# Kernel tuning notes

Hardware: AMD Instinct MI355X
Metric: run time of the kernel (lower is better)

## Reference

```python
import jax, jax.numpy as jnp
import numpy as np

B, TQ, TK, DQ, DK = 8, 2048, 2048, 512, 512


def setup_inputs() -> dict:
    key = jax.random.key(0)
    kq, kk, kv, km, kw = jax.random.split(key, 5)
    q = jax.random.normal(kq, (B, TQ, DQ), dtype=jnp.float32)
    k = jax.random.normal(kk, (B, TK, DK), dtype=jnp.float32)
    v = jax.random.normal(kv, (B, TK, DK), dtype=jnp.float32)
    attn_mask = jax.random.randint(km, (B, TQ, TK), 0, 2) > 0
    # xavier_uniform for (DQ, DK)
    limit = float(np.sqrt(6.0 / (DQ + DK)))
    weights = jax.random.uniform(kw, (DQ, DK), minval=-limit, maxval=limit, dtype=jnp.float32)
    return {"q": q, "k": k, "v": v, "attn_mask": attn_mask, "weights": weights}


def reference(q, k, v, attn_mask, weights):
    # scores: (B, TQ, TK) = (q @ W) @ k^T
    qw = jnp.einsum('bqd,de->bqe', q, weights)
    scores = jnp.einsum('bqe,bke->bqk', qw, k)
    scores = jnp.where(attn_mask, -jnp.inf, scores)
    attention = jax.nn.softmax(scores, axis=-1)
    # dropout_rate = 0.0 -> identity
    output = jnp.einsum('bqk,bkd->bqd', attention, v)
    return (output, attention)
```

## Files before the change

kernel.cpp:

```cpp
#include <hip/hip_runtime.h>
#include <stdint.h>

#define TQs 2048
#define TKs 2048
#define DDs 512
#define NBs 8

typedef float f32x4 __attribute__((ext_vector_type(4)));
typedef short bf16x8 __attribute__((ext_vector_type(8)));
typedef short bf16x4 __attribute__((ext_vector_type(4)));
typedef _Float16 half8 __attribute__((ext_vector_type(8)));

__device__ __forceinline__ unsigned short f2bf(float x){
  unsigned u = __float_as_uint(x);
  return (unsigned short)((u + 0x7fffu + ((u>>16)&1u)) >> 16);
}
__device__ __forceinline__ float bf2f(unsigned short h){
  return __uint_as_float(((unsigned)h)<<16);
}

__device__ __forceinline__ void gload16(const void* g, void* l){
  __builtin_amdgcn_global_load_lds(
      (const __attribute__((address_space(1))) unsigned int*)(unsigned long long)(uintptr_t)g,
      (__attribute__((address_space(3))) unsigned int*)(unsigned int)(uintptr_t)l,
      16, 0, 0);
}

__global__ __launch_bounds__(256) void k0_kf(const float* __restrict__ kk, _Float16* __restrict__ kf){
  const long n8 = (long)NBs*TKs*DDs/8;
  for(long i = (long)blockIdx.x*256 + threadIdx.x; i < n8; i += (long)gridDim.x*256){
    f32x4 x0 = ((const f32x4*)kk)[2*i];
    f32x4 x1 = ((const f32x4*)kk)[2*i+1];
    half8 h;
    #pragma unroll
    for(int j=0;j<4;j++){ h[j] = (_Float16)x0[j]; h[4+j] = (_Float16)x1[j]; }
    ((half8*)kf)[i] = h;
  }
}

__global__ __launch_bounds__(256) void k0_transpose_v(const float* __restrict__ v, short* __restrict__ vt){
  __shared__ float tile[64][65];
  int b = blockIdx.z;
  int t0 = blockIdx.x*64, d0 = blockIdx.y*64;
  int tid = threadIdx.x;
  int r = tid>>2, cs = (tid&3)*16;
  const float* src = v + ((long)b*TKs + t0 + r)*DDs + d0 + cs;
  #pragma unroll
  for(int i=0;i<4;i++){
    f32x4 x = ((const f32x4*)src)[i];
    tile[r][cs+4*i+0]=x[0]; tile[r][cs+4*i+1]=x[1]; tile[r][cs+4*i+2]=x[2]; tile[r][cs+4*i+3]=x[3];
  }
  __syncthreads();
  int dr = tid>>2, ts = (tid&3)*16;
  bf16x8 b0, b1;
  #pragma unroll
  for(int i=0;i<8;i++){ b0[i] = (short)f2bf(tile[ts+i][dr]); b1[i] = (short)f2bf(tile[ts+8+i][dr]); }
  short* dst = vt + ((long)b*DDs + d0 + dr)*TKs + t0 + ts;
  ((bf16x8*)dst)[0] = b0;
  ((bf16x8*)dst)[1] = b1;
}

__global__ __launch_bounds__(256) void k0_wt(const float* __restrict__ wsrc,
                                             short* __restrict__ wth, short* __restrict__ wtl){
  __shared__ float tile[64][65];
  int d0 = blockIdx.x*64, e0 = blockIdx.y*64;
  int tid = threadIdx.x;
  int r = tid>>2, cs = (tid&3)*16;
  const float* src = wsrc + ((long)(d0 + r))*DDs + e0 + cs;
  #pragma unroll
  for(int i=0;i<4;i++){
    f32x4 x = ((const f32x4*)src)[i];
    tile[r][cs+4*i+0]=x[0]; tile[r][cs+4*i+1]=x[1]; tile[r][cs+4*i+2]=x[2]; tile[r][cs+4*i+3]=x[3];
  }
  __syncthreads();
  int er = tid>>2, ds = (tid&3)*16;
  bf16x8 h0,h1,l0,l1;
  #pragma unroll
  for(int i=0;i<8;i++){
    float x = tile[ds+i][er];
    unsigned short hh = f2bf(x);
    h0[i] = (short)hh; l0[i] = (short)f2bf(x - bf2f(hh));
  }
  #pragma unroll
  for(int i=0;i<8;i++){
    float x = tile[ds+8+i][er];
    unsigned short hh = f2bf(x);
    h1[i] = (short)hh; l1[i] = (short)f2bf(x - bf2f(hh));
  }
  short* dh = wth + ((long)(e0+er))*DDs + d0 + ds;
  short* dl = wtl + ((long)(e0+er))*DDs + d0 + ds;
  ((bf16x8*)dh)[0] = h0; ((bf16x8*)dh)[1] = h1;
  ((bf16x8*)dl)[0] = l0; ((bf16x8*)dl)[1] = l1;
}

__global__ __launch_bounds__(256,2) void k1_qw(const float* __restrict__ q,
                                               const short* __restrict__ wth, const short* __restrict__ wtl,
                                               _Float16* __restrict__ qwh, _Float16* __restrict__ qwl){
  __shared__ short qah[8192], qal[8192];
  __shared__ short wbh[8192], wbl[8192];
  int q0 = blockIdx.x*128, e0 = blockIdx.y*128;
  int tid = threadIdx.x, lane = tid&63, w4 = tid>>6;
  int wm = w4>>1, wn = w4&1;
  int i15 = lane&15, g4 = lane>>4;
  f32x4 acc[4][4];
  #pragma unroll
  for(int a=0;a<4;a++)
    #pragma unroll
    for(int bq=0;bq<4;bq++) acc[a][bq] = (f32x4){0.f,0.f,0.f,0.f};
  for(int k0=0;k0<DDs;k0+=64){
    __syncthreads();
    #pragma unroll
    for(int j=0;j<4;j++){
      int J = j*4 + w4;
      long so = (long)(e0 + (J>>1)*16 + i15)*DDs + k0 + ((J&1)*4 + g4)*8;
      gload16(wth + so, &wbh[J*512]);
      gload16(wtl + so, &wbl[J*512]);
    }
    #pragma unroll
    for(int j=0;j<4;j++){
      int c = j*256 + tid;
      int ci = c&15, cg = (c>>4)&3, cks = (c>>6)&1, crb = c>>7;
      const float* s = q + (long)(q0 + crb*16 + ci)*DDs + k0 + (cks*4+cg)*8;
      f32x4 x0 = ((const f32x4*)s)[0];
      f32x4 x1 = ((const f32x4*)s)[1];
      bf16x8 h, l;
      #pragma unroll
      for(int jj=0;jj<4;jj++){
        unsigned short hj = f2bf(x0[jj]);
        h[jj] = (short)hj; l[jj] = (short)f2bf(x0[jj]-bf2f(hj));
      }
      #pragma unroll
      for(int jj=0;jj<4;jj++){
        unsigned short hj = f2bf(x1[jj]);
        h[4+jj] = (short)hj; l[4+jj] = (short)f2bf(x1[jj]-bf2f(hj));
      }
      *(bf16x8*)&qah[c*8] = h;
      *(bf16x8*)&qal[c*8] = l;
    }
    __syncthreads();
    #pragma unroll
    for(int ks=0;ks<2;ks++){
      bf16x8 a_h[4], a_l[4], b_h[4], b_l[4];
      #pragma unroll
      for(int mf=0;mf<4;mf++){
        int c = ((wm*4+mf)*2+ks)*64 + lane;
        a_h[mf] = *(const bf16x8*)&qah[c*8];
        a_l[mf] = *(const bf16x8*)&qal[c*8];
      }
      #pragma unroll
      for(int nf=0;nf<4;nf++){
        int c = ((wn*4+nf)*2+ks)*64 + lane;
        b_h[nf] = *(const bf16x8*)&wbh[c*8];
        b_l[nf] = *(const bf16x8*)&wbl[c*8];
      }
      #pragma unroll
      for(int mf=0;mf<4;mf++)
      #pragma unroll
      for(int nf=0;nf<4;nf++){
        acc[mf][nf] = __builtin_amdgcn_mfma_f32_16x16x32_bf16(a_h[mf], b_h[nf], acc[mf][nf],0,0,0);
        acc[mf][nf] = __builtin_amdgcn_mfma_f32_16x16x32_bf16(a_h[mf], b_l[nf], acc[mf][nf],0,0,0);
        acc[mf][nf] = __builtin_amdgcn_mfma_f32_16x16x32_bf16(a_l[mf], b_h[nf], acc[mf][nf],0,0,0);
      }
    }
  }
  int rr = g4*4, cc = i15;
  #pragma unroll
  for(int mf=0;mf<4;mf++)
  #pragma unroll
  for(int nf=0;nf<4;nf++)
  #pragma unroll
  for(int r2=0;r2<4;r2++){
    long row = q0 + wm*64 + mf*16 + rr + r2;
    long col = e0 + wn*64 + nf*16 + cc;
    float s = acc[mf][nf][r2];
    _Float16 h = (_Float16)s;
    qwh[row*DDs + col] = h;
    qwl[row*DDs + col] = (_Float16)(s - (float)h);
  }
}

__global__ __launch_bounds__(256,2) void k2a(const _Float16* __restrict__ qwh, const _Float16* __restrict__ qwl,
                                             const _Float16* __restrict__ kf,
                                             const int* __restrict__ mask, float* __restrict__ attn,
                                             float* __restrict__ m_ws, float* __restrict__ l_ws){
  __shared__ _Float16 kb[2][16384];
  int rb = blockIdx.x;
  int chunk = blockIdx.y;
  int tid = threadIdx.x, lane = tid&63, w = tid>>6;
  int b = rb>>5;
  long qrow0 = (long)rb*64 + w*16;
  int i15 = lane&15, g4 = lane>>4;
  half8 ah[16], al[16];
  {
    const _Float16* ph = qwh + (qrow0 + i15)*DDs + g4*8;
    const _Float16* pl = qwl + (qrow0 + i15)*DDs + g4*8;
    #pragma unroll
    for(int kc=0;kc<16;kc++){
      ah[kc] = *(const half8*)(ph + kc*32);
      al[kc] = *(const half8*)(pl + kc*32);
    }
  }
  float m_st[4], l_st[4];
  #pragma unroll
  for(int r=0;r<4;r++){ m_st[r]=-1e30f; l_st[r]=0.f; }
  const _Float16* kbase = kf + (long)b*TKs*DDs;
  {
    int t0 = chunk*512;
    #pragma unroll
    for(int j=0;j<8;j++){
      int J = j*4 + w;
      long so = (long)(t0 + ((J>>4)<<4) + i15)*DDs + (J&15)*32 + g4*8;
      gload16(kbase + so, &kb[0][J*512]);
    }
  }
  __syncthreads();
  int cur = 0;
  for(int it=0; it<16; ++it){
    int t0 = chunk*512 + it*32;
    if(it < 15){
      int t1 = t0 + 32;
      #pragma unroll
      for(int j=0;j<8;j++){
        int J = j*4 + w;
        long so = (long)(t1 + ((J>>4)<<4) + i15)*DDs + (J&15)*32 + g4*8;
        gload16(kbase + so, &kb[cur^1][J*512]);
      }
    }
    int mv[2][4];
    #pragma unroll
    for(int nf=0;nf<2;nf++)
      #pragma unroll
      for(int r=0;r<4;r++)
        mv[nf][r] = mask[(qrow0 + g4*4 + r)*TKs + t0 + nf*16 + i15];
    f32x4 acc[2];
    acc[0]=(f32x4){0.f,0.f,0.f,0.f}; acc[1]=(f32x4){0.f,0.f,0.f,0.f};
    #pragma unroll
    for(int ks=0;ks<16;ks++){
      #pragma unroll
      for(int nf=0;nf<2;nf++){
        half8 bh = *(const half8*)&kb[cur][((nf*16+ks)*64 + lane)*8];
        acc[nf] = __builtin_amdgcn_mfma_f32_16x16x32_f16(ah[ks], bh, acc[nf],0,0,0);
        acc[nf] = __builtin_amdgcn_mfma_f32_16x16x32_f16(al[ks], bh, acc[nf],0,0,0);
      }
    }
    #pragma unroll
    for(int r=0;r<4;r++){
      float s0 = acc[0][r];
      float s1 = acc[1][r];
      if(mv[0][r]) s0 = -3e38f;
      if(mv[1][r]) s1 = -3e38f;
      float mo = m_st[r];
      float mn = fmaxf(mo, fmaxf(s0,s1));
      l_st[r] = l_st[r]*__expf(mo-mn) + __expf(s0-mn) + __expf(s1-mn);
      m_st[r] = mn;
      long row = qrow0 + g4*4 + r;
      attn[row*TKs + t0 + i15] = s0;
      attn[row*TKs + t0 + 16 + i15] = s1;
    }
    __syncthreads();
    cur ^= 1;
  }
  #pragma unroll
  for(int r=0;r<4;r++){
    #pragma unroll
    for(int d=1; d<16; d<<=1){
      float m2 = __shfl_xor(m_st[r], d, 16);
      float l2 = __shfl_xor(l_st[r], d, 16);
      float mn = fmaxf(m_st[r], m2);
      l_st[r] = l_st[r]*__expf(m_st[r]-mn) + l2*__expf(m2-mn);
      m_st[r] = mn;
    }
  }
  if(i15==0){
    #pragma unroll
    for(int r=0;r<4;r++){
      long row = qrow0 + g4*4 + r;
      m_ws[row*4 + chunk] = m_st[r];
      l_ws[row*4 + chunk] = l_st[r];
    }
  }
}

__global__ __launch_bounds__(256,2) void k2b(const short* __restrict__ vt, const float* __restrict__ m_ws,
                                             const float* __restrict__ l_ws, float* __restrict__ attn,
                                             float* __restrict__ outp){
  __shared__ short vf[2][16384];
  __shared__ short at2[2][2048];
  __shared__ float ms[64], rls[64];
  int rb = blockIdx.x;
  long row0 = (long)rb*64;
  int b = rb>>5;
  int tid=threadIdx.x, lane=tid&63, w=tid>>6;
  int i15 = lane&15, g4 = lane>>4;
  const short* vb = vt + (long)b*DDs*TKs;
  float* arow = attn + row0*TKs;
  int r_ = tid>>2, t8w = tid&3;
  #pragma unroll
  for(int j=0;j<8;j++){
    int J = j*4 + w;
    long so = (long)(J*16 + i15)*TKs + g4*8;
    gload16(vb + so, &vf[0][J*512]);
  }
  if(tid < 64){
    long row = row0 + tid;
    float m0=m_ws[row*4+0], m1=m_ws[row*4+1], m2=m_ws[row*4+2], m3=m_ws[row*4+3];
    float M = fmaxf(fmaxf(m0,m1),fmaxf(m2,m3));
    float L = l_ws[row*4+0]*__expf(m0-M) + l_ws[row*4+1]*__expf(m1-M)
            + l_ws[row*4+2]*__expf(m2-M) + l_ws[row*4+3]*__expf(m3-M);
    ms[tid] = M;
    rls[tid] = 1.0f/L;
  }
  __syncthreads();
  {
    float* p = arow + (long)r_*TKs + t8w*8;
    f32x4 s0v = ((const f32x4*)p)[0];
    f32x4 s1v = ((const f32x4*)p)[1];
    float M = ms[r_], RL = rls[r_];
    f32x4 a0, a1;
    #pragma unroll
    for(int j=0;j<4;j++){ a0[j] = __expf(s0v[j]-M)*RL; a1[j] = __expf(s1v[j]-M)*RL; }
    ((f32x4*)p)[0] = a0;
    ((f32x4*)p)[1] = a1;
    bf16x8 ab;
    #pragma unroll
    for(int j=0;j<4;j++){ ab[j] = (short)f2bf(a0[j]); ab[4+j] = (short)f2bf(a1[j]); }
    int cell = ((r_>>4)<<6) + (t8w<<4) + (r_&15);
    *(bf16x8*)&at2[0][cell*8] = ab;
  }
  __syncthreads();
  f32x4 acc[4][8];
  #pragma unroll
  for(int mf=0;mf<4;mf++)
    #pragma unroll
    for(int nf=0;nf<8;nf++) acc[mf][nf]=(f32x4){0.f,0.f,0.f,0.f};
  int c = 0;
  for(int it=0; it<64; ++it){
    f32x4 s0v, s1v;
    if(it < 63){
      int t1 = (it+1)*32;
      #pragma unroll
      for(int j=0;j<8;j++){
        int J = j*4 + w;
        long so = (long)(J*16 + i15)*TKs + t1 + g4*8;
        gload16(vb + so, &vf[c^1][J*512]);
      }
      float* p = arow + (long)r_*TKs + t1 + t8w*8;
      s0v = ((const f32x4*)p)[0];
      s1v = ((const f32x4*)p)[1];
    }
    bf16x8 af[4], bfr[8];
    #pragma unroll
    for(int mf=0;mf<4;mf++) af[mf] = *(const bf16x8*)&at2[c][(mf*64 + lane)*8];
    #pragma unroll
    for(int nf=0;nf<8;nf++) bfr[nf] = *(const bf16x8*)&vf[c][((w*8+nf)*64 + lane)*8];
    #pragma unroll
    for(int mf=0;mf<4;mf++)
    #pragma unroll
    for(int nf=0;nf<8;nf++)
      acc[mf][nf] = __builtin_amdgcn_mfma_f32_16x16x32_bf16(af[mf], bfr[nf], acc[mf][nf],0,0,0);
    if(it < 63){
      int t1 = (it+1)*32;
      float* p = arow + (long)r_*TKs + t1 + t8w*8;
      float M = ms[r_], RL = rls[r_];
      f32x4 a0, a1;
      #pragma unroll
      for(int j=0;j<4;j++){ a0[j] = __expf(s0v[j]-M)*RL; a1[j] = __expf(s1v[j]-M)*RL; }
      ((f32x4*)p)[0] = a0;
      ((f32x4*)p)[1] = a1;
      bf16x8 ab;
      #pragma unroll
      for(int j=0;j<4;j++){ ab[j] = (short)f2bf(a0[j]); ab[4+j] = (short)f2bf(a1[j]); }
      int cell = ((r_>>4)<<6) + (t8w<<4) + (r_&15);
      *(bf16x8*)&at2[c^1][cell*8] = ab;
    }
    __syncthreads();
    c ^= 1;
  }
  #pragma unroll
  for(int mf=0;mf<4;mf++)
  #pragma unroll
  for(int nf=0;nf<8;nf++)
  #pragma unroll
  for(int r2=0;r2<4;r2++){
    long row = row0 + mf*16 + g4*4 + r2;
    long col = w*128 + nf*16 + i15;
    outp[row*DDs + col] = acc[mf][nf][r2];
  }
}

extern "C" void kernel_launch(void* const* d_in, const int* in_sizes, int n_in,
                              void* d_out, int out_size, void* d_ws, size_t ws_size,
                              hipStream_t stream) {
  const float* q    = (const float*)d_in[0];
  const float* k    = (const float*)d_in[1];
  const float* v    = (const float*)d_in[2];
  const int*   mask = (const int*)d_in[3];
  const float* wsrc = (const float*)d_in[4];
  float* outp = (float*)d_out;
  float* attn = (float*)d_out + (long)NBs*TQs*DDs;
  char* ws = (char*)d_ws;
  const long NE = (long)NBs*TKs*DDs;
  _Float16* kf  = (_Float16*)ws;
  short*    vt  = (short*)(ws + 2*NE);
  _Float16* qwh = (_Float16*)(ws + 4*NE);
  _Float16* qwl = (_Float16*)(ws + 6*NE);
  float* m_ws = (float*)(ws + 8*NE);
  float* l_ws = (float*)(ws + 8*NE + 65536*4);
  short* wth = (short*)attn;
  short* wtl = (short*)attn + 262144;
  hipLaunchKernelGGL(k0_kf,          dim3(1024),    dim3(256), 0, stream, k, kf);
  hipLaunchKernelGGL(k0_transpose_v, dim3(32,8,8),  dim3(256), 0, stream, v, vt);
  hipLaunchKernelGGL(k0_wt,          dim3(8,8),     dim3(256), 0, stream, wsrc, wth, wtl);
  hipLaunchKernelGGL(k1_qw,          dim3(128,4),   dim3(256), 0, stream, q, wth, wtl, qwh, qwl);
  hipLaunchKernelGGL(k2a,            dim3(256,4),   dim3(256), 0, stream, qwh, qwl, kf, mask, attn, m_ws, l_ws);
  hipLaunchKernelGGL(k2b,            dim3(256),     dim3(256), 0, stream, vt, m_ws, l_ws, attn, outp);
}
```

Measured before the change: 321.1 us.

## Shrink k2a key tile and split k2b into smaller row blocks for occupancy

k2a now processes 16 keys per iteration instead of 32, which halves its LDS tile and raises launch bounds to 3 blocks per CU. It keeps separate hi/lo accumulators to shorten the MFMA dependency chain. k2b now uses 32-row blocks with 512 threads and a grid of 512 blocks, so the grid covers more CUs and each warp holds fewer accumulators. The cost is more loop iterations and barriers in k2a, and V tiles reloaded by twice as many blocks in k2b.

Result: slower. 485.6 us (+51.2%).

```diff
diff --git a/kernel.cpp b/kernel.cpp
--- a/kernel.cpp
+++ b/kernel.cpp
@@ -179,11 +179,11 @@
   }
 }
 
-__global__ __launch_bounds__(256,2) void k2a(const _Float16* __restrict__ qwh, const _Float16* __restrict__ qwl,
+__global__ __launch_bounds__(256,3) void k2a(const _Float16* __restrict__ qwh, const _Float16* __restrict__ qwl,
                                              const _Float16* __restrict__ kf,
                                              const int* __restrict__ mask, float* __restrict__ attn,
                                              float* __restrict__ m_ws, float* __restrict__ l_ws){
-  __shared__ _Float16 kb[2][16384];
+  __shared__ _Float16 kb[2][8192];
   int rb = blockIdx.x;
   int chunk = blockIdx.y;
   int tid = threadIdx.x, lane = tid&63, w = tid>>6;
@@ -207,55 +207,46 @@
   {
     int t0 = chunk*512;
     #pragma unroll
-    for(int j=0;j<8;j++){
+    for(int j=0;j<4;j++){
       int J = j*4 + w;
-      long so = (long)(t0 + ((J>>4)<<4) + i15)*DDs + (J&15)*32 + g4*8;
+      long so = (long)(t0 + i15)*DDs + J*32 + g4*8;
       gload16(kbase + so, &kb[0][J*512]);
     }
   }
   __syncthreads();
   int cur = 0;
-  for(int it=0; it<16; ++it){
-    int t0 = chunk*512 + it*32;
-    if(it < 15){
-      int t1 = t0 + 32;
-      #pragma unroll
-      for(int j=0;j<8;j++){
+  for(int it=0; it<32; ++it){
+    int t0 = chunk*512 + it*16;
+    if(it < 31){
+      int t1 = t0 + 16;
+      #pragma unroll
+      for(int j=0;j<4;j++){
         int J = j*4 + w;
-        long so = (long)(t1 + ((J>>4)<<4) + i15)*DDs + (J&15)*32 + g4*8;
+        long so = (long)(t1 + i15)*DDs + J*32 + g4*8;
         gload16(kbase + so, &kb[cur^1][J*512]);
       }
     }
-    int mv[2][4];
-    #pragma unroll
-    for(int nf=0;nf<2;nf++)
-      #pragma unroll
-      for(int r=0;r<4;r++)
-        mv[nf][r] = mask[(qrow0 + g4*4 + r)*TKs + t0 + nf*16 + i15];
-    f32x4 acc[2];
-    acc[0]=(f32x4){0.f,0.f,0.f,0.f}; acc[1]=(f32x4){0.f,0.f,0.f,0.f};
+    int mv[4];
+    #pragma unroll
+    for(int r=0;r<4;r++)
+      mv[r] = mask[(qrow0 + g4*4 + r)*TKs + t0 + i15];
+    f32x4 acch = (f32x4){0.f,0.f,0.f,0.f};
+    f32x4 accl = (f32x4){0.f,0.f,0.f,0.f};
     #pragma unroll
     for(int ks=0;ks<16;ks++){
-      #pragma unroll
-      for(int nf=0;nf<2;nf++){
-        half8 bh = *(const half8*)&kb[cur][((nf*16+ks)*64 + lane)*8];
-        acc[nf] = __builtin_amdgcn_mfma_f32_16x16x32_f16(ah[ks], bh, acc[nf],0,0,0);
-        acc[nf] = __builtin_amdgcn_mfma_f32_16x16x32_f16(al[ks], bh, acc[nf],0,0,0);
-      }
+      half8 bh = *(const half8*)&kb[cur][ks*512 + lane*8];
+      acch = __builtin_amdgcn_mfma_f32_16x16x32_f16(ah[ks], bh, acch,0,0,0);
+      accl = __builtin_amdgcn_mfma_f32_16x16x32_f16(al[ks], bh, accl,0,0,0);
     }
     #pragma unroll
     for(int r=0;r<4;r++){
-      float s0 = acc[0][r];
-      float s1 = acc[1][r];
-      if(mv[0][r]) s0 = -3e38f;
-      if(mv[1][r]) s1 = -3e38f;
+      float s = acch[r] + accl[r];
+      if(mv[r]) s = -3e38f;
       float mo = m_st[r];
-      float mn = fmaxf(mo, fmaxf(s0,s1));
-      l_st[r] = l_st[r]*__expf(mo-mn) + __expf(s0-mn) + __expf(s1-mn);
+      float mn = fmaxf(mo, s);
+      l_st[r] = l_st[r]*__expf(mo-mn) + __expf(s-mn);
       m_st[r] = mn;
-      long row = qrow0 + g4*4 + r;
-      attn[row*TKs + t0 + i15] = s0;
-      attn[row*TKs + t0 + 16 + i15] = s1;
+      attn[(qrow0 + g4*4 + r)*TKs + t0 + i15] = s;
     }
     __syncthreads();
     cur ^= 1;
@@ -281,27 +272,26 @@
   }
 }
 
-__global__ __launch_bounds__(256,2) void k2b(const short* __restrict__ vt, const float* __restrict__ m_ws,
+__global__ __launch_bounds__(512,4) void k2b(const short* __restrict__ vt, const float* __restrict__ m_ws,
                                              const float* __restrict__ l_ws, float* __restrict__ attn,
                                              float* __restrict__ outp){
   __shared__ short vf[2][16384];
-  __shared__ short at2[2][2048];
-  __shared__ float ms[64], rls[64];
+  __shared__ short at2[2][1024];
+  __shared__ float ms[32], rls[32];
   int rb = blockIdx.x;
-  long row0 = (long)rb*64;
-  int b = rb>>5;
+  long row0 = (long)rb*32;
+  int b = rb>>6;
   int tid=threadIdx.x, lane=tid&63, w=tid>>6;
   int i15 = lane&15, g4 = lane>>4;
   const short* vb = vt + (long)b*DDs*TKs;
   float* arow = attn + row0*TKs;
-  int r_ = tid>>2, t8w = tid&3;
-  #pragma unroll
-  for(int j=0;j<8;j++){
-    int J = j*4 + w;
+  #pragma unroll
+  for(int j=0;j<4;j++){
+    int J = j*8 + w;
     long so = (long)(J*16 + i15)*TKs + g4*8;
     gload16(vb + so, &vf[0][J*512]);
   }
-  if(tid < 64){
+  if(tid < 32){
     long row = row0 + tid;
     float m0=m_ws[row*4+0], m1=m_ws[row*4+1], m2=m_ws[row*4+2], m3=m_ws[row*4+3];
     float M = fmaxf(fmaxf(m0,m1),fmaxf(m2,m3));
@@ -311,8 +301,9 @@
     rls[tid] = 1.0f/L;
   }
   __syncthreads();
-  {
-    float* p = arow + (long)r_*TKs + t8w*8;
+  if(tid < 128){
+    int r_ = tid>>2, tg = tid&3;
+    float* p = arow + (long)r_*TKs + tg*8;
     f32x4 s0v = ((const f32x4*)p)[0];
     f32x4 s1v = ((const f32x4*)p)[1];
     float M = ms[r_], RL = rls[r_];
@@ -324,43 +315,46 @@
     bf16x8 ab;
     #pragma unroll
     for(int j=0;j<4;j++){ ab[j] = (short)f2bf(a0[j]); ab[4+j] = (short)f2bf(a1[j]); }
-    int cell = ((r_>>4)<<6) + (t8w<<4) + (r_&15);
-    *(bf16x8*)&at2[0][cell*8] = ab;
+    int cell = r_>>4, lfr = (r_&15) | (tg<<4);
+    *(bf16x8*)&at2[0][(cell*64 + lfr)*8] = ab;
   }
   __syncthreads();
-  f32x4 acc[4][8];
-  #pragma unroll
-  for(int mf=0;mf<4;mf++)
-    #pragma unroll
-    for(int nf=0;nf<8;nf++) acc[mf][nf]=(f32x4){0.f,0.f,0.f,0.f};
+  f32x4 acc[2][4];
+  #pragma unroll
+  for(int mf=0;mf<2;mf++)
+    #pragma unroll
+    for(int nf=0;nf<4;nf++) acc[mf][nf]=(f32x4){0.f,0.f,0.f,0.f};
   int c = 0;
   for(int it=0; it<64; ++it){
     f32x4 s0v, s1v;
+    int r_ = tid>>2, tg = tid&3;
     if(it < 63){
       int t1 = (it+1)*32;
       #pragma unroll
-      for(int j=0;j<8;j++){
-        int J = j*4 + w;
+      for(int j=0;j<4;j++){
+        int J = j*8 + w;
         long so = (long)(J*16 + i15)*TKs + t1 + g4*8;
         gload16(vb + so, &vf[c^1][J*512]);
       }
-      float* p = arow + (long)r_*TKs + t1 + t8w*8;
-      s0v = ((const f32x4*)p)[0];
-      s1v = ((const f32x4*)p)[1];
-    }
-    bf16x8 af[4], bfr[8];
-    #pragma unroll
-    for(int mf=0;mf<4;mf++) af[mf] = *(const bf16x8*)&at2[c][(mf*64 + lane)*8];
-    #pragma unroll
-    for(int nf=0;nf<8;nf++) bfr[nf] = *(const bf16x8*)&vf[c][((w*8+nf)*64 + lane)*8];
-    #pragma unroll
-    for(int mf=0;mf<4;mf++)
-    #pragma unroll
-    for(int nf=0;nf<8;nf++)
+      if(tid < 128){
+        const float* p = arow + (long)r_*TKs + t1 + tg*8;
+        s0v = ((const f32x4*)p)[0];
+        s1v = ((const f32x4*)p)[1];
+      }
+    }
+    bf16x8 af[2], bfr[4];
+    #pragma unroll
+    for(int mf=0;mf<2;mf++) af[mf] = *(const bf16x8*)&at2[c][(mf*64 + lane)*8];
+    #pragma unroll
+    for(int nf=0;nf<4;nf++) bfr[nf] = *(const bf16x8*)&vf[c][((w*4+nf)*64 + lane)*8];
+    #pragma unroll
+    for(int mf=0;mf<2;mf++)
+    #pragma unroll
+    for(int nf=0;nf<4;nf++)
       acc[mf][nf] = __builtin_amdgcn_mfma_f32_16x16x32_bf16(af[mf], bfr[nf], acc[mf][nf],0,0,0);
-    if(it < 63){
+    if(it < 63 && tid < 128){
       int t1 = (it+1)*32;
-      float* p = arow + (long)r_*TKs + t1 + t8w*8;
+      float* p = arow + (long)r_*TKs + t1 + tg*8;
       float M = ms[r_], RL = rls[r_];
       f32x4 a0, a1;
       #pragma unroll
@@ -370,20 +364,20 @@
       bf16x8 ab;
       #pragma unroll
       for(int j=0;j<4;j++){ ab[j] = (short)f2bf(a0[j]); ab[4+j] = (short)f2bf(a1[j]); }
-      int cell = ((r_>>4)<<6) + (t8w<<4) + (r_&15);
-      *(bf16x8*)&at2[c^1][cell*8] = ab;
+      int cell = r_>>4, lfr = (r_&15) | (tg<<4);
+      *(bf16x8*)&at2[c^1][(cell*64 + lfr)*8] = ab;
     }
     __syncthreads();
     c ^= 1;
   }
   #pragma unroll
-  for(int mf=0;mf<4;mf++)
-  #pragma unroll
-  for(int nf=0;nf<8;nf++)
+  for(int mf=0;mf<2;mf++)
+  #pragma unroll
+  for(int nf=0;nf<4;nf++)
   #pragma unroll
   for(int r2=0;r2<4;r2++){
     long row = row0 + mf*16 + g4*4 + r2;
-    long col = w*128 + nf*16 + i15;
+    long col = w*64 + nf*16 + i15;
     outp[row*DDs + col] = acc[mf][nf][r2];
   }
 }
@@ -413,5 +407,5 @@
   hipLaunchKernelGGL(k0_wt,          dim3(8,8),     dim3(256), 0, stream, wsrc, wth, wtl);
   hipLaunchKernelGGL(k1_qw,          dim3(128,4),   dim3(256), 0, stream, q, wth, wtl, qwh, qwl);
   hipLaunchKernelGGL(k2a,            dim3(256,4),   dim3(256), 0, stream, qwh, qwl, kf, mask, attn, m_ws, l_ws);
-  hipLaunchKernelGGL(k2b,            dim3(256),     dim3(256), 0, stream, vt, m_ws, l_ws, attn, outp);
-}
+  hipLaunchKernelGGL(k2b,            dim3(512),     dim3(512), 0, stream, vt, m_ws, l_ws, attn, outp);
+}
```
